# Kernel tuning notes

Measured on AMD Instinct MI355X. Metric: run time of the kernel, lower is better.

The kernel has to match this reference:

```python
import jax, jax.numpy as jnp
import numpy as np

B, L, C = 64, 4096, 16
PL, PC, NP, D, FS = 128, 8, 64, 64, 100  # patch_size_L, patch_size_C, num_patches, output_dim, f_s


def setup_inputs() -> dict:
    key = jax.random.key(0)
    ks = jax.random.split(key, 9)
    x = jax.random.normal(ks[0], (B, L, C), dtype=jnp.float32)
    start_L = jax.random.randint(ks[1], (B, NP), 0, L - PL + 1, dtype=jnp.int32)
    idx_C = jax.random.randint(ks[2], (B, NP, PC), 0, C, dtype=jnp.int32)
    W1 = jax.random.normal(ks[3], (2 * PC + 1, D), dtype=jnp.float32) * 0.2
    b1 = jax.random.normal(ks[4], (D,), dtype=jnp.float32) * 0.02
    W2 = jax.random.normal(ks[5], (2 * D + 1, D), dtype=jnp.float32) * 0.1
    b2 = jax.random.normal(ks[6], (D,), dtype=jnp.float32) * 0.02
    W3 = jax.random.normal(ks[7], (PL * D, D), dtype=jnp.float32) * 0.01
    b3 = jax.random.normal(ks[8], (D,), dtype=jnp.float32) * 0.02
    return dict(x=x, start_L=start_L, idx_C=idx_C, W1=W1, b1=b1, W2=W2, b2=b2, W3=W3, b3=b3)


def reference(x, start_L, idx_C, W1, b1, W2, b2, W3, b3):
    T = 1.0 / FS
    # contiguous window indices along L (wrapped), [B, NP, PL]
    idx_L = (start_L[:, :, None] + jnp.arange(PL, dtype=jnp.int32)) % L
    # fused double gather: avoid materializing the [B, NP, L, C] broadcast of the original
    bidx = jnp.arange(B)[:, None, None, None]
    patches = x[bidx, idx_L[:, :, :, None], idx_C[:, :, None, :]]        # [B, NP, PL, PC]
    # time embedding: t = arange(L)*T gathered by idx_L
    t_patches = (idx_L.astype(jnp.float32) * T)[..., None]               # [B, NP, PL, 1]
    # channel embedding: c = arange(C) gathered by idx_C
    c_patches = jnp.broadcast_to(idx_C.astype(jnp.float32)[:, :, None, :], (B, NP, PL, PC))
    feats = jnp.concatenate([patches, t_patches, c_patches], axis=-1)    # [B, NP, PL, 2*PC+1]
    h = jax.nn.silu(feats @ W1 + b1)                                     # [B, NP, PL, D]
    # --- fft branch (computed then discarded by the original module; kept for fidelity) ---
    f = jnp.linspace(0.0, FS / 2.0, PL // 2 + 1)
    fft = jnp.fft.rfft(h, axis=-2, norm='ortho')                         # [B, NP, PL//2+1, D]
    f_patches = jnp.broadcast_to(f[None, None, :, None], (B, NP, PL // 2 + 1, 1))
    fcat = jnp.concatenate([fft.real, fft.imag, f_patches], axis=-1)     # [B, NP, PL//2+1, 2D+1]
    _unused = jax.nn.silu(fcat @ W2 + b2)
    # --- mixer on flattened patches ---
    flat = h.reshape(B, NP, PL * D)                                      # [B, NP, PL*D]
    out = jax.nn.silu(flat @ W3 + b3)                                    # [B, NP, D]
    return out
```

## Files before the change

### kernel.cpp

```cpp
#include <hip/hip_runtime.h>
#include <hip/hip_bf16.h>

#define BB 64
#define LL 4096
#define CC 16
#define PL 128
#define PC 8
#define NPP 64
#define DD 64
#define TSTEP 0.01f

#define PPB 16
#define KSPLIT 8
#define LT_PER (PL / KSPLIT)
#define NT_MAIN 256
#define XSTRIDE 12

typedef float f32x4 __attribute__((ext_vector_type(4)));
typedef int   i32x4 __attribute__((ext_vector_type(4)));
typedef unsigned int u32;

__device__ __forceinline__ u32 f2bf(float f) {
    u32 u = __float_as_uint(f);
    return (u + 0x7fffu + ((u >> 16) & 1u)) >> 16;
}
__device__ __forceinline__ float silu_f(float z) {
    return z * __builtin_amdgcn_rcpf(1.0f + __expf(-z));
}
__device__ __forceinline__ u32 pack_bf16(float lo, float hi) {
    __hip_bfloat162 p = __float22bfloat162_rn(float2{lo, hi});
    u32 r;
    __builtin_memcpy(&r, &p, 4);
    return r;
}

__global__ __launch_bounds__(256) void w3_prep(const float* __restrict__ W3,
                                               u32* __restrict__ wsf) {
    const int tid  = blockIdx.x * 256 + threadIdx.x;
    const int lane = tid & 63;
    const int m    = tid >> 6;
    const int ns   = m & 3;
    const int kb   = (m >> 2) * 32;
    const int row0 = kb + ((lane >> 4) << 3);
    const int col  = (ns << 4) + (lane & 15);
    u32 q[4];
    #pragma unroll
    for (int jj = 0; jj < 4; ++jj) {
        const float lo = W3[(size_t)(row0 + 2 * jj)     * DD + col];
        const float hi = W3[(size_t)(row0 + 2 * jj + 1) * DD + col];
        q[jj] = f2bf(lo) | (f2bf(hi) << 16);
    }
    i32x4 v; v.x = q[0]; v.y = q[1]; v.z = q[2]; v.w = q[3];
    *(i32x4*)(wsf + (size_t)m * 256 + (lane << 2)) = v;
}

template<bool USE_WS>
__global__ __launch_bounds__(NT_MAIN) void htfe_main(
    const float* __restrict__ x, const int* __restrict__ start_L,
    const int* __restrict__ idx_C, const float* __restrict__ W1,
    const float* __restrict__ b1, const float* __restrict__ W3,
    const u32* __restrict__ wsf, float* __restrict__ out)
{
    __shared__ __align__(16) float xvbuf[LT_PER][PPB * XSTRIDE];
    __shared__ __align__(16) u32   hbuf[2][PPB * DD / 2];
    __shared__ int sStart[PPB];
    __shared__ int sCi[PPB][PC];

    const int t    = threadIdx.x;
    const int lane = t & 63;
    const int w    = t >> 6;
    const int blk  = blockIdx.x;
    const int split = blk & (KSPLIT - 1);
    const int mb    = blk >> 3;
    const int b     = mb >> 2;
    const int p0    = (mb & 3) * PPB;
    const int lt0   = split * LT_PER;

    if (t < PPB) sStart[t] = start_L[b * NPP + p0 + t];
    if (t < PPB * PC) {
        const int pp = t >> 3, c = t & 7;
        sCi[pp][c] = idx_C[(size_t)((b * NPP + p0 + pp) << 3) + c];
    }
    __syncthreads();

    const int p  = lane >> 2;
    const int d0 = (w << 4) + ((lane & 3) << 2);
    float w1x[PC][4], w1t[4], cb[4];
    {
        const f32x4 vt = *(const f32x4*)(W1 + PC * DD + d0);
        const f32x4 vb = *(const f32x4*)(b1 + d0);
        const float st = (float)sStart[p] * TSTEP;
        #pragma unroll
        for (int j = 0; j < 4; ++j) { w1t[j] = vt[j]; cb[j] = vb[j] + st * vt[j]; }
        #pragma unroll
        for (int c = 0; c < PC; ++c) {
            const f32x4 vx = *(const f32x4*)(W1 + c * DD + d0);
            const f32x4 vc = *(const f32x4*)(W1 + (PC + 1 + c) * DD + d0);
            const float cf = (float)sCi[p][c];
            #pragma unroll
            for (int j = 0; j < 4; ++j) { w1x[c][j] = vx[j]; cb[j] += cf * vc[j]; }
        }
    }

    for (int i = t; i < LT_PER * PPB * PC; i += NT_MAIN) {
        const int lt = i >> 7;
        const int pp = (i >> 3) & 15;
        const int c  = i & 7;
        xvbuf[lt][pp * XSTRIDE + c] =
            x[((size_t)b * LL + (size_t)(sStart[pp] + lt0 + lt)) * CC + sCi[pp][c]];
    }
    __syncthreads();

    const int wrByte = ((p << 7) + (d0 << 1)) ^ ((p & 7) << 4);
    const int pB    = lane & 15;
    const int rbase = (pB << 7) + ((lane >> 4) << 4);
    const int swzB  = (pB & 7) << 4;
    const int rd0 = rbase ^ swzB;
    const int rd1 = (rbase + 64) ^ swzB;

    f32x4 acc = {0.f, 0.f, 0.f, 0.f};
    const u32* bsrc = wsf + (size_t)(lt0 * 8 + w) * 256 + (lane << 2);

    for (int lt = 0; lt < LT_PER; ++lt) {
        const int cur = lt & 1;
        const float tl = (float)(lt0 + lt) * TSTEP;
        const float* xvp = &xvbuf[lt][p * XSTRIDE];
        const f32x4 xa = *(const f32x4*)xvp;
        const f32x4 xc = *(const f32x4*)(xvp + 4);
        float hh[4];
        #pragma unroll
        for (int j = 0; j < 4; ++j) {
            float a = cb[j] + tl * w1t[j];
            a += xa.x * w1x[0][j]; a += xa.y * w1x[1][j];
            a += xa.z * w1x[2][j]; a += xa.w * w1x[3][j];
            a += xc.x * w1x[4][j]; a += xc.y * w1x[5][j];
            a += xc.z * w1x[6][j]; a += xc.w * w1x[7][j];
            hh[j] = silu_f(a);
        }
        const u32 pk0 = pack_bf16(hh[0], hh[1]);
        const u32 pk1 = pack_bf16(hh[2], hh[3]);
        char* hbB = (char*)&hbuf[cur][0];
        *(uint2*)(hbB + wrByte) = make_uint2(pk0, pk1);

        i32x4 bf0, bf1;
        if (USE_WS) {
            bf0 = *(const i32x4*)(bsrc);
            bf1 = *(const i32x4*)(bsrc + 1024);
            bsrc += 2048;
        } else {
            const int row0 = (lt0 + lt) * DD + ((lane >> 4) << 3);
            const int colW = (w << 4) + pB;
            u32 q[8];
            #pragma unroll
            for (int jj = 0; jj < 4; ++jj) {
                q[jj]     = f2bf(W3[(size_t)(row0 + 2*jj)      * DD + colW]) |
                            (f2bf(W3[(size_t)(row0 + 2*jj + 1) * DD + colW]) << 16);
                q[4 + jj] = f2bf(W3[(size_t)(row0 + 32 + 2*jj)      * DD + colW]) |
                            (f2bf(W3[(size_t)(row0 + 32 + 2*jj + 1) * DD + colW]) << 16);
            }
            bf0.x = q[0]; bf0.y = q[1]; bf0.z = q[2]; bf0.w = q[3];
            bf1.x = q[4]; bf1.y = q[5]; bf1.z = q[6]; bf1.w = q[7];
        }

        __syncthreads();

        const i32x4 af0 = *(const i32x4*)(hbB + rd0);
        const i32x4 af1 = *(const i32x4*)(hbB + rd1);
        if (!USE_WS) asm volatile("s_nop 3" ::);
        asm("v_mfma_f32_16x16x32_bf16 %0, %1, %2, %0" : "+v"(acc) : "v"(af0), "v"(bf0));
        asm("v_mfma_f32_16x16x32_bf16 %0, %1, %2, %0" : "+v"(acc) : "v"(af1), "v"(bf1));
    }

    asm volatile("s_nop 7\ns_nop 7\ns_nop 7" ::);
    #pragma unroll
    for (int r = 0; r < 4; ++r) {
        const int prow = ((lane >> 4) << 2) + r;
        atomicAdd(out + (size_t)(b * NPP + p0 + prow) * DD + (w << 4) + pB, acc[r]);
    }
}

__global__ __launch_bounds__(256) void finish_silu(float* __restrict__ out,
                                                   const float* __restrict__ b3) {
    const int i = blockIdx.x * 256 + threadIdx.x;
    const int base = i << 2;
    f32x4 v = *(f32x4*)(out + base);
    const f32x4 bb = *(const f32x4*)(b3 + (base & 63));
    #pragma unroll
    for (int j = 0; j < 4; ++j) v[j] = silu_f(v[j] + bb[j]);
    *(f32x4*)(out + base) = v;
}

extern "C" void kernel_launch(void* const* d_in, const int* in_sizes, int n_in,
                              void* d_out, int out_size, void* d_ws, size_t ws_size,
                              hipStream_t stream) {
    const float* x       = (const float*)d_in[0];
    const int*   start_L = (const int*)  d_in[1];
    const int*   idx_C   = (const int*)  d_in[2];
    const float* W1      = (const float*)d_in[3];
    const float* b1      = (const float*)d_in[4];
    const float* W3      = (const float*)d_in[7];
    const float* b3      = (const float*)d_in[8];
    float* out = (float*)d_out;
    u32*   wsf = (u32*)d_ws;

    (void)hipMemsetAsync(d_out, 0, (size_t)out_size * sizeof(float), stream);

    const int grid_main = BB * (NPP / PPB) * KSPLIT;
    const bool use_ws = ws_size >= (size_t)(PL * 2 * 4) * 1024;
    if (use_ws) {
        w3_prep<<<256, 256, 0, stream>>>(W3, wsf);
        htfe_main<true><<<grid_main, NT_MAIN, 0, stream>>>(
            x, start_L, idx_C, W1, b1, W3, wsf, out);
    } else {
        htfe_main<false><<<grid_main, NT_MAIN, 0, stream>>>(
            x, start_L, idx_C, W1, b1, W3, wsf, out);
    }
    finish_silu<<<(BB * NPP * DD / 4) / 256, 256, 0, stream>>>(out, b3);
}
```

Measured before the change: 39.92 us.

## Use 32x32 MFMA tiles with 32 patches per block and deterministic split reduction

Doubles the patches per block to 32 and switches to 32x32x16 bf16 MFMA, with waves split across N halves and K halves plus an in-block LDS reduction. The gathered x values are packed to bf16 in shared memory. Global atomics and the memset are replaced by per-split partial buffers, summed in a separate finish_reduce kernel that also applies bias and SiLU. This aims to improve MFMA efficiency and remove atomic contention, at the cost of extra workspace traffic for the partials and halving the grid size.

```diff
diff --git a/kernel.cpp b/kernel.cpp
--- a/kernel.cpp
+++ b/kernel.cpp
@@ -10,20 +10,21 @@
 #define DD 64
 #define TSTEP 0.01f
 
-#define PPB 16
+#define PPB 32
 #define KSPLIT 8
 #define LT_PER (PL / KSPLIT)
 #define NT_MAIN 256
-#define XSTRIDE 12
-
-typedef float f32x4 __attribute__((ext_vector_type(4)));
-typedef int   i32x4 __attribute__((ext_vector_type(4)));
+#define NMB (BB * (NPP / PPB))
+
+#define FRAG_U32 (PL * 8 * 256)
+#define PART_FLT (KSPLIT * NMB * 2 * 64 * 16)
+#define SPLIT_STRIDE (NMB * 2 * 64 * 16)
+
+typedef float f32x4  __attribute__((ext_vector_type(4)));
+typedef float f32x16 __attribute__((ext_vector_type(16)));
+typedef int   i32x4  __attribute__((ext_vector_type(4)));
 typedef unsigned int u32;
 
-__device__ __forceinline__ u32 f2bf(float f) {
-    u32 u = __float_as_uint(f);
-    return (u + 0x7fffu + ((u >> 16) & 1u)) >> 16;
-}
 __device__ __forceinline__ float silu_f(float z) {
     return z * __builtin_amdgcn_rcpf(1.0f + __expf(-z));
 }
@@ -39,41 +40,43 @@
     const int tid  = blockIdx.x * 256 + threadIdx.x;
     const int lane = tid & 63;
     const int m    = tid >> 6;
-    const int ns   = m & 3;
-    const int kb   = (m >> 2) * 32;
-    const int row0 = kb + ((lane >> 4) << 3);
-    const int col  = (ns << 4) + (lane & 15);
+    const int ns   = m & 1;
+    const int ksub = (m >> 1) & 1;
+    const int kk   = (m >> 2) & 1;
+    const int ltg  = m >> 3;
+    const int k0   = ltg * 64 + kk * 32 + ksub * 16 + ((lane >> 5) << 3);
+    const int col  = (ns << 5) + (lane & 31);
     u32 q[4];
     #pragma unroll
-    for (int jj = 0; jj < 4; ++jj) {
-        const float lo = W3[(size_t)(row0 + 2 * jj)     * DD + col];
-        const float hi = W3[(size_t)(row0 + 2 * jj + 1) * DD + col];
-        q[jj] = f2bf(lo) | (f2bf(hi) << 16);
-    }
-    i32x4 v; v.x = q[0]; v.y = q[1]; v.z = q[2]; v.w = q[3];
+    for (int jj = 0; jj < 4; ++jj)
+        q[jj] = pack_bf16(W3[(size_t)(k0 + 2 * jj)     * DD + col],
+                          W3[(size_t)(k0 + 2 * jj + 1) * DD + col]);
+    i32x4 v; v.x = (int)q[0]; v.y = (int)q[1]; v.z = (int)q[2]; v.w = (int)q[3];
     *(i32x4*)(wsf + (size_t)m * 256 + (lane << 2)) = v;
 }
 
-template<bool USE_WS>
 __global__ __launch_bounds__(NT_MAIN) void htfe_main(
     const float* __restrict__ x, const int* __restrict__ start_L,
     const int* __restrict__ idx_C, const float* __restrict__ W1,
-    const float* __restrict__ b1, const float* __restrict__ W3,
-    const u32* __restrict__ wsf, float* __restrict__ out)
+    const float* __restrict__ b1, const u32* __restrict__ wsf,
+    float* __restrict__ part)
 {
-    __shared__ __align__(16) float xvbuf[LT_PER][PPB * XSTRIDE];
-    __shared__ __align__(16) u32   hbuf[2][PPB * DD / 2];
+    __shared__ __align__(16) u32   xq[LT_PER][PPB][4];
+    __shared__ __align__(16) u32   hbuf[2][PPB][32];
+    __shared__ __align__(16) float redbuf[2][64][16];
     __shared__ int sStart[PPB];
     __shared__ int sCi[PPB][PC];
 
     const int t    = threadIdx.x;
     const int lane = t & 63;
     const int w    = t >> 6;
-    const int blk  = blockIdx.x;
-    const int split = blk & (KSPLIT - 1);
-    const int mb    = blk >> 3;
-    const int b     = mb >> 2;
-    const int p0    = (mb & 3) * PPB;
+    const int ns   = w & 1;
+    const int kk   = w >> 1;
+
+    const int mb    = blockIdx.x & (NMB - 1);
+    const int split = blockIdx.x >> 7;
+    const int b     = mb >> 1;
+    const int p0    = (mb & 1) * PPB;
     const int lt0   = split * LT_PER;
 
     if (t < PPB) sStart[t] = start_L[b * NPP + p0 + t];
@@ -83,111 +86,154 @@
     }
     __syncthreads();
 
-    const int p  = lane >> 2;
-    const int d0 = (w << 4) + ((lane & 3) << 2);
-    float w1x[PC][4], w1t[4], cb[4];
+    const int pA  = lane >> 2;
+    const int pB2 = pA + 16;
+    const int d0  = (w << 4) + ((lane & 3) << 2);
+    float w1x[PC][4], w1t[4], cbA[4], cbB[4];
     {
         const f32x4 vt = *(const f32x4*)(W1 + PC * DD + d0);
         const f32x4 vb = *(const f32x4*)(b1 + d0);
-        const float st = (float)sStart[p] * TSTEP;
-        #pragma unroll
-        for (int j = 0; j < 4; ++j) { w1t[j] = vt[j]; cb[j] = vb[j] + st * vt[j]; }
+        const float stA = (float)sStart[pA]  * TSTEP;
+        const float stB = (float)sStart[pB2] * TSTEP;
+        #pragma unroll
+        for (int j = 0; j < 4; ++j) {
+            w1t[j] = vt[j];
+            cbA[j] = vb[j] + stA * vt[j];
+            cbB[j] = vb[j] + stB * vt[j];
+        }
         #pragma unroll
         for (int c = 0; c < PC; ++c) {
             const f32x4 vx = *(const f32x4*)(W1 + c * DD + d0);
             const f32x4 vc = *(const f32x4*)(W1 + (PC + 1 + c) * DD + d0);
-            const float cf = (float)sCi[p][c];
+            const float cfA = (float)sCi[pA][c];
+            const float cfB = (float)sCi[pB2][c];
             #pragma unroll
-            for (int j = 0; j < 4; ++j) { w1x[c][j] = vx[j]; cb[j] += cf * vc[j]; }
-        }
-    }
-
-    for (int i = t; i < LT_PER * PPB * PC; i += NT_MAIN) {
-        const int lt = i >> 7;
-        const int pp = (i >> 3) & 15;
-        const int c  = i & 7;
-        xvbuf[lt][pp * XSTRIDE + c] =
-            x[((size_t)b * LL + (size_t)(sStart[pp] + lt0 + lt)) * CC + sCi[pp][c]];
+            for (int j = 0; j < 4; ++j) {
+                w1x[c][j] = vx[j];
+                cbA[j] += cfA * vc[j];
+                cbB[j] += cfB * vc[j];
+            }
+        }
+    }
+
+    #pragma unroll
+    for (int uu = 0; uu < 2; ++uu) {
+        const int u  = t * 2 + uu;
+        const int lt = u >> 5;
+        const int pp = u & 31;
+        const float* xrow = x + ((size_t)b * LL + (size_t)(sStart[pp] + lt0 + lt)) * CC;
+        u32 q[4];
+        #pragma unroll
+        for (int c2 = 0; c2 < 4; ++c2)
+            q[c2] = pack_bf16(xrow[sCi[pp][2 * c2]], xrow[sCi[pp][2 * c2 + 1]]);
+        i32x4 v; v.x = (int)q[0]; v.y = (int)q[1]; v.z = (int)q[2]; v.w = (int)q[3];
+        *(i32x4*)&xq[lt][pp][0] = v;
     }
     __syncthreads();
 
-    const int wrByte = ((p << 7) + (d0 << 1)) ^ ((p & 7) << 4);
-    const int pB    = lane & 15;
-    const int rbase = (pB << 7) + ((lane >> 4) << 4);
-    const int swzB  = (pB & 7) << 4;
-    const int rd0 = rbase ^ swzB;
-    const int rd1 = (rbase + 64) ^ swzB;
-
-    f32x4 acc = {0.f, 0.f, 0.f, 0.f};
-    const u32* bsrc = wsf + (size_t)(lt0 * 8 + w) * 256 + (lane << 2);
+    const int wrA = (pA << 7) + (((w << 5) + ((lane & 3) << 3)) ^ ((pA & 7) << 4));
+    const int aRow = (lane & 31) << 7;
+    const int aSwz = (lane & 7) << 4;
+    const int cb0  = (kk << 6) + ((lane >> 5) << 4);
+    const int aOff0 = aRow + (cb0 ^ aSwz);
+    const int aOff1 = aRow + ((cb0 + 32) ^ aSwz);
+
+    f32x16 acc = {};
+    const u32* bsrc = wsf + ((size_t)lt0 * 8 + kk * 4 + ns) * 256 + (lane << 2);
 
     for (int lt = 0; lt < LT_PER; ++lt) {
         const int cur = lt & 1;
+
+        const i32x4 bf0 = *(const i32x4*)(bsrc);
+        const i32x4 bf1 = *(const i32x4*)(bsrc + 512);
+        bsrc += 2048;
+
         const float tl = (float)(lt0 + lt) * TSTEP;
-        const float* xvp = &xvbuf[lt][p * XSTRIDE];
-        const f32x4 xa = *(const f32x4*)xvp;
-        const f32x4 xc = *(const f32x4*)(xvp + 4);
-        float hh[4];
+        const i32x4 qa = *(const i32x4*)&xq[lt][pA][0];
+        const i32x4 qb = *(const i32x4*)&xq[lt][pB2][0];
+        float aA[4], aB[4];
         #pragma unroll
         for (int j = 0; j < 4; ++j) {
-            float a = cb[j] + tl * w1t[j];
-            a += xa.x * w1x[0][j]; a += xa.y * w1x[1][j];
-            a += xa.z * w1x[2][j]; a += xa.w * w1x[3][j];
-            a += xc.x * w1x[4][j]; a += xc.y * w1x[5][j];
-            a += xc.z * w1x[6][j]; a += xc.w * w1x[7][j];
-            hh[j] = silu_f(a);
-        }
-        const u32 pk0 = pack_bf16(hh[0], hh[1]);
-        const u32 pk1 = pack_bf16(hh[2], hh[3]);
-        char* hbB = (char*)&hbuf[cur][0];
-        *(uint2*)(hbB + wrByte) = make_uint2(pk0, pk1);
-
-        i32x4 bf0, bf1;
-        if (USE_WS) {
-            bf0 = *(const i32x4*)(bsrc);
-            bf1 = *(const i32x4*)(bsrc + 1024);
-            bsrc += 2048;
-        } else {
-            const int row0 = (lt0 + lt) * DD + ((lane >> 4) << 3);
-            const int colW = (w << 4) + pB;
-            u32 q[8];
+            aA[j] = cbA[j] + tl * w1t[j];
+            aB[j] = cbB[j] + tl * w1t[j];
+        }
+        #pragma unroll
+        for (int c2 = 0; c2 < 4; ++c2) {
+            const u32 ua = (u32)qa[c2], ub = (u32)qb[c2];
+            const float xa0 = __uint_as_float(ua << 16);
+            const float xa1 = __uint_as_float(ua & 0xffff0000u);
+            const float xb0 = __uint_as_float(ub << 16);
+            const float xb1 = __uint_as_float(ub & 0xffff0000u);
             #pragma unroll
-            for (int jj = 0; jj < 4; ++jj) {
-                q[jj]     = f2bf(W3[(size_t)(row0 + 2*jj)      * DD + colW]) |
-                            (f2bf(W3[(size_t)(row0 + 2*jj + 1) * DD + colW]) << 16);
-                q[4 + jj] = f2bf(W3[(size_t)(row0 + 32 + 2*jj)      * DD + colW]) |
-                            (f2bf(W3[(size_t)(row0 + 32 + 2*jj + 1) * DD + colW]) << 16);
+            for (int j = 0; j < 4; ++j) {
+                aA[j] += xa0 * w1x[2 * c2][j];
+                aA[j] += xa1 * w1x[2 * c2 + 1][j];
+                aB[j] += xb0 * w1x[2 * c2][j];
+                aB[j] += xb1 * w1x[2 * c2 + 1][j];
             }
-            bf0.x = q[0]; bf0.y = q[1]; bf0.z = q[2]; bf0.w = q[3];
-            bf1.x = q[4]; bf1.y = q[5]; bf1.z = q[6]; bf1.w = q[7];
-        }
+        }
+        char* hb = (char*)&hbuf[cur][0][0];
+        *(uint2*)(hb + wrA) =
+            make_uint2(pack_bf16(silu_f(aA[0]), silu_f(aA[1])),
+                       pack_bf16(silu_f(aA[2]), silu_f(aA[3])));
+        *(uint2*)(hb + wrA + 2048) =
+            make_uint2(pack_bf16(silu_f(aB[0]), silu_f(aB[1])),
+                       pack_bf16(silu_f(aB[2]), silu_f(aB[3])));
 
         __syncthreads();
 
-        const i32x4 af0 = *(const i32x4*)(hbB + rd0);
-        const i32x4 af1 = *(const i32x4*)(hbB + rd1);
-        if (!USE_WS) asm volatile("s_nop 3" ::);
-        asm("v_mfma_f32_16x16x32_bf16 %0, %1, %2, %0" : "+v"(acc) : "v"(af0), "v"(bf0));
-        asm("v_mfma_f32_16x16x32_bf16 %0, %1, %2, %0" : "+v"(acc) : "v"(af1), "v"(bf1));
+        const i32x4 af0 = *(const i32x4*)(hb + aOff0);
+        const i32x4 af1 = *(const i32x4*)(hb + aOff1);
+        asm("v_mfma_f32_32x32x16_bf16 %0, %1, %2, %0" : "+v"(acc) : "v"(af0), "v"(bf0));
+        asm("v_mfma_f32_32x32x16_bf16 %0, %1, %2, %0" : "+v"(acc) : "v"(af1), "v"(bf1));
     }
 
     asm volatile("s_nop 7\ns_nop 7\ns_nop 7" ::);
-    #pragma unroll
-    for (int r = 0; r < 4; ++r) {
-        const int prow = ((lane >> 4) << 2) + r;
-        atomicAdd(out + (size_t)(b * NPP + p0 + prow) * DD + (w << 4) + pB, acc[r]);
-    }
-}
-
-__global__ __launch_bounds__(256) void finish_silu(float* __restrict__ out,
-                                                   const float* __restrict__ b3) {
-    const int i = blockIdx.x * 256 + threadIdx.x;
-    const int base = i << 2;
-    f32x4 v = *(f32x4*)(out + base);
-    const f32x4 bb = *(const f32x4*)(b3 + (base & 63));
-    #pragma unroll
-    for (int j = 0; j < 4; ++j) v[j] = silu_f(v[j] + bb[j]);
-    *(f32x4*)(out + base) = v;
+    if (kk) {
+        #pragma unroll
+        for (int r4 = 0; r4 < 4; ++r4) {
+            f32x4 v;
+            v.x = acc[r4 * 4 + 0]; v.y = acc[r4 * 4 + 1];
+            v.z = acc[r4 * 4 + 2]; v.w = acc[r4 * 4 + 3];
+            *(f32x4*)&redbuf[ns][lane][r4 * 4] = v;
+        }
+    }
+    __syncthreads();
+    if (!kk) {
+        float* pdst = part + ((((size_t)split * NMB + mb) * 2 + ns) * 64 + lane) * 16;
+        #pragma unroll
+        for (int r4 = 0; r4 < 4; ++r4) {
+            const f32x4 v = *(const f32x4*)&redbuf[ns][lane][r4 * 4];
+            f32x4 o;
+            o.x = acc[r4 * 4 + 0] + v.x; o.y = acc[r4 * 4 + 1] + v.y;
+            o.z = acc[r4 * 4 + 2] + v.z; o.w = acc[r4 * 4 + 3] + v.w;
+            *(f32x4*)(pdst + r4 * 4) = o;
+        }
+    }
+}
+
+__global__ __launch_bounds__(256) void finish_reduce(const float* __restrict__ part,
+                                                     const float* __restrict__ b3,
+                                                     float* __restrict__ out) {
+    const int tid  = blockIdx.x * 256 + threadIdx.x;
+    const int rq   = tid & 3;
+    const int lane = (tid >> 2) & 63;
+    const int ns   = (tid >> 8) & 1;
+    const int mb   = tid >> 9;
+    const float* src = part + (((size_t)mb * 2 + ns) * 64 + lane) * 16 + rq * 4;
+    f32x4 s = {0.f, 0.f, 0.f, 0.f};
+    #pragma unroll
+    for (int split = 0; split < KSPLIT; ++split) {
+        const f32x4 v = *(const f32x4*)(src + (size_t)split * SPLIT_STRIDE);
+        s.x += v.x; s.y += v.y; s.z += v.z; s.w += v.w;
+    }
+    const int col  = (ns << 5) + (lane & 31);
+    const float bias = b3[col];
+    #pragma unroll
+    for (int j = 0; j < 4; ++j) {
+        const int prow = j + 8 * rq + 4 * (lane >> 5);
+        out[(size_t)(mb * 32 + prow) * DD + col] = silu_f(s[j] + bias);
+    }
 }
 
 extern "C" void kernel_launch(void* const* d_in, const int* in_sizes, int n_in,
@@ -200,20 +246,11 @@
     const float* b1      = (const float*)d_in[4];
     const float* W3      = (const float*)d_in[7];
     const float* b3      = (const float*)d_in[8];
-    float* out = (float*)d_out;
-    u32*   wsf = (u32*)d_ws;
-
-    (void)hipMemsetAsync(d_out, 0, (size_t)out_size * sizeof(float), stream);
-
-    const int grid_main = BB * (NPP / PPB) * KSPLIT;
-    const bool use_ws = ws_size >= (size_t)(PL * 2 * 4) * 1024;
-    if (use_ws) {
-        w3_prep<<<256, 256, 0, stream>>>(W3, wsf);
-        htfe_main<true><<<grid_main, NT_MAIN, 0, stream>>>(
-            x, start_L, idx_C, W1, b1, W3, wsf, out);
-    } else {
-        htfe_main<false><<<grid_main, NT_MAIN, 0, stream>>>(
-            x, start_L, idx_C, W1, b1, W3, wsf, out);
-    }
-    finish_silu<<<(BB * NPP * DD / 4) / 256, 256, 0, stream>>>(out, b3);
-}
+    float* out  = (float*)d_out;
+    u32*   wsf  = (u32*)d_ws;
+    float* part = (float*)(wsf + FRAG_U32);
+
+    w3_prep<<<256, 256, 0, stream>>>(W3, wsf);
+    htfe_main<<<NMB * KSPLIT, NT_MAIN, 0, stream>>>(x, start_L, idx_C, W1, b1, wsf, part);
+    finish_reduce<<<256, 256, 0, stream>>>(part, b3, out);
+}
```

New measurement: 40.23 us. Within noise of the previous version (+0.8%).
